# Optimization experiments

Hardware: AMD Instinct MI355X
Metric: run time of the kernel (lower is better)

Reference implementation:

```python
import jax, jax.numpy as jnp
import numpy as np

ALPHA = 1.0
BETA = 10.0
MARGIN = 0.5


def setup_inputs() -> dict:
    key = jax.random.key(0)
    k1, k2 = jax.random.split(key)
    emb = jax.random.normal(k1, (4096, 512), dtype=jnp.float32)
    # module docstring: embeddings are L2-normalized
    emb = emb / jnp.linalg.norm(emb, axis=1, keepdims=True)
    labels = jax.random.randint(k2, (4096,), 0, 64, dtype=jnp.int64)
    return {"embeddings": emb, "labels": labels}


def reference(embeddings, labels):
    n = embeddings.shape[0]
    sim = embeddings @ embeddings.T  # [n, n]
    labels_eq = labels[None, :] == labels[:, None]
    eye = jnp.eye(n, dtype=bool)
    pos_mask = labels_eq & ~eye
    neg_mask = ~labels_eq & ~eye

    # masked exp-sums (masked entries contribute 0, matching torch's
    # clone/NEG_INF/zero-out dance without materializing extra copies)
    pos_exp = jnp.where(pos_mask, jnp.exp(-ALPHA * (sim - MARGIN)), 0.0)
    neg_exp = jnp.where(neg_mask, jnp.exp(BETA * (sim - MARGIN)), 0.0)
    pos_term = (1.0 / ALPHA) * jnp.log1p(pos_exp.sum(axis=1))
    neg_term = (1.0 / BETA) * jnp.log1p(neg_exp.sum(axis=1))

    valid = pos_mask.any(axis=1) & neg_mask.any(axis=1)
    n_valid = valid.sum()
    total = jnp.where(valid, pos_term + neg_term, 0.0).sum()
    return jnp.where(n_valid > 0, total / jnp.maximum(n_valid, 1).astype(sim.dtype), 0.0)
```

## Files before the change

kernel.cpp:

```cpp
#include <hip/hip_runtime.h>
#include <hip/hip_bf16.h>

#define N 4096
#define D 512
#define MARGIN 0.5f
#define BETA 10.0f

typedef __attribute__((ext_vector_type(8))) short short8;
typedef __attribute__((ext_vector_type(4))) float floatx4;

__device__ inline unsigned short f2bf(float f) {
    unsigned u = __float_as_uint(f);
    u += 0x7fffu + ((u >> 16) & 1u);
    return (unsigned short)(u >> 16);
}

__global__ void convert_bf16_kernel(const float4* __restrict__ in,
                                    ushort4* __restrict__ out) {
    int idx = blockIdx.x * 256 + threadIdx.x;
    float4 v = in[idx];
    ushort4 o;
    o.x = f2bf(v.x); o.y = f2bf(v.y); o.z = f2bf(v.z); o.w = f2bf(v.w);
    out[idx] = o;
}

__global__ void ms_loss_gemm(const unsigned short* __restrict__ Ebf,
                             const int* __restrict__ labels,
                             float* __restrict__ pos_sum,
                             float* __restrict__ neg_sum) {
    __shared__ unsigned short Atile[128 * 32];
    __shared__ unsigned short Btile[128 * 32];
    __shared__ int rlab[128];
    __shared__ int clab[128];

    const int tid  = threadIdx.x;
    const int wave = tid >> 6;
    const int lane = tid & 63;
    const int quad = lane >> 4;
    const int lcol = lane & 15;
    const int wrow = wave >> 1;
    const int wcol = wave & 1;
    const int ibase = blockIdx.y * 128;
    const int jbase = blockIdx.x * 128;

    if (tid < 128)       rlab[tid]       = labels[ibase + tid];
    else                 clab[tid - 128] = labels[jbase + tid - 128];

    floatx4 acc[4][4];
#pragma unroll
    for (int mt = 0; mt < 4; ++mt)
#pragma unroll
        for (int nt = 0; nt < 4; ++nt)
            acc[mt][nt] = (floatx4){0.f, 0.f, 0.f, 0.f};

    const char* Eb = (const char*)Ebf;
    char* Ab = (char*)Atile;
    char* Bb = (char*)Btile;
    const int srow = lane >> 2;
    const int skb  = (lane & 3) * 16;

    for (int kt = 0; kt < D / 32; ++kt) {
        __syncthreads();
        const int kb = kt * 64;
#pragma unroll
        for (int it = 0; it < 2; ++it) {
            int r    = wave * 16 + it * 64 + srow;
            int ldso = wave * 1024 + it * 4096 + lane * 16;
            const char* ga = Eb + (size_t)(ibase + r) * (D * 2) + kb + skb;
            const char* gb = Eb + (size_t)(jbase + r) * (D * 2) + kb + skb;
            __builtin_amdgcn_global_load_lds(
                (const __attribute__((address_space(1))) void*)ga,
                (__attribute__((address_space(3))) void*)(Ab + ldso), 16, 0, 0);
            __builtin_amdgcn_global_load_lds(
                (const __attribute__((address_space(1))) void*)gb,
                (__attribute__((address_space(3))) void*)(Bb + ldso), 16, 0, 0);
        }
        __syncthreads();

        short8 a[4], b[4];
#pragma unroll
        for (int mt = 0; mt < 4; ++mt) {
            int r = wrow * 64 + mt * 16 + lcol;
            a[mt] = *(const short8*)(Ab + r * 64 + quad * 16);
        }
#pragma unroll
        for (int nt = 0; nt < 4; ++nt) {
            int c = wcol * 64 + nt * 16 + lcol;
            b[nt] = *(const short8*)(Bb + c * 64 + quad * 16);
        }
#pragma unroll
        for (int mt = 0; mt < 4; ++mt)
#pragma unroll
            for (int nt = 0; nt < 4; ++nt)
                acc[mt][nt] = __builtin_amdgcn_mfma_f32_16x16x32_bf16(
                    a[mt], b[nt], acc[mt][nt], 0, 0, 0);
    }

    float pacc[16], nacc[16];
#pragma unroll
    for (int t = 0; t < 16; ++t) { pacc[t] = 0.f; nacc[t] = 0.f; }

#pragma unroll
    for (int mt = 0; mt < 4; ++mt) {
#pragma unroll
        for (int nt = 0; nt < 4; ++nt) {
            int cl = wcol * 64 + nt * 16 + lcol;
            int gj = jbase + cl;
            int lj = clab[cl];
#pragma unroll
            for (int reg = 0; reg < 4; ++reg) {
                int rl = wrow * 64 + mt * 16 + quad * 4 + reg;
                int gi = ibase + rl;
                float s = acc[mt][nt][reg];
                if (gi != gj) {
                    if (rlab[rl] == lj)
                        pacc[mt * 4 + reg] += __expf(MARGIN - s);
                    else
                        nacc[mt * 4 + reg] += __expf(BETA * (s - MARGIN));
                }
            }
        }
    }

#pragma unroll
    for (int t = 0; t < 16; ++t) {
        float p = pacc[t], ng = nacc[t];
        p += __shfl_xor(p, 1);  ng += __shfl_xor(ng, 1);
        p += __shfl_xor(p, 2);  ng += __shfl_xor(ng, 2);
        p += __shfl_xor(p, 4);  ng += __shfl_xor(ng, 4);
        p += __shfl_xor(p, 8);  ng += __shfl_xor(ng, 8);
        if (lcol == 0) {
            int mt = t >> 2, reg = t & 3;
            int gi = ibase + wrow * 64 + mt * 16 + quad * 4 + reg;
            atomicAdd(&pos_sum[gi], p);
            atomicAdd(&neg_sum[gi], ng);
        }
    }
}

__global__ void finalize_kernel(const float* __restrict__ pos_sum,
                                const float* __restrict__ neg_sum,
                                float* __restrict__ out) {
    __shared__ float sb[256];
    __shared__ int   sc[256];
    const int tid = threadIdx.x;
    float tot = 0.f;
    int cnt = 0;
    for (int i = tid; i < N; i += 256) {
        float p = pos_sum[i], ng = neg_sum[i];
        if (p > 0.f && ng > 0.f) {
            tot += log1pf(p) + (1.0f / BETA) * log1pf(ng);
            cnt += 1;
        }
    }
    sb[tid] = tot; sc[tid] = cnt;
    __syncthreads();
    for (int s = 128; s > 0; s >>= 1) {
        if (tid < s) { sb[tid] += sb[tid + s]; sc[tid] += sc[tid + s]; }
        __syncthreads();
    }
    if (tid == 0) out[0] = (sc[0] > 0) ? sb[0] / (float)sc[0] : 0.f;
}

extern "C" void kernel_launch(void* const* d_in, const int* in_sizes, int n_in,
                              void* d_out, int out_size, void* d_ws, size_t ws_size,
                              hipStream_t stream) {
    const float* emb   = (const float*)d_in[0];
    const int* labels  = (const int*)d_in[1];
    float* out         = (float*)d_out;

    char* ws = (char*)d_ws;
    unsigned short* Ebf = (unsigned short*)ws;
    float* pos_sum = (float*)(ws + (size_t)N * D * 2);
    float* neg_sum = pos_sum + N;

    hipMemsetAsync(pos_sum, 0, 2 * N * sizeof(float), stream);

    convert_bf16_kernel<<<(N * D / 4) / 256, 256, 0, stream>>>(
        (const float4*)emb, (ushort4*)Ebf);

    dim3 grid(N / 128, N / 128);
    ms_loss_gemm<<<grid, 256, 0, stream>>>(Ebf, labels, pos_sum, neg_sum);

    finalize_kernel<<<1, 256, 0, stream>>>(pos_sum, neg_sum, out);
}
```

Measured before the change: 104.5 us.

## Swizzle LDS tiles, fuse zeroing into convert, restructure epilogue and finalize

XOR-swizzles the 16-byte k-chunks on both the global-to-LDS staging and the MFMA fragment reads, to reduce LDS bank conflicts. Drops the separate memset by zeroing the sum buffers inside the bf16 conversion kernel. Reorders the epilogue so each row's partial sums are reduced and committed right away instead of held in 32 accumulators, which lowers register pressure. Also adds launch bounds and vectorizes the finalize loads with float4.

```diff
diff --git a/kernel.cpp b/kernel.cpp
--- a/kernel.cpp
+++ b/kernel.cpp
@@ -15,19 +15,22 @@
     return (unsigned short)(u >> 16);
 }
 
-__global__ void convert_bf16_kernel(const float4* __restrict__ in,
-                                    ushort4* __restrict__ out) {
+__global__ __launch_bounds__(256) void convert_bf16_kernel(
+        const float4* __restrict__ in, ushort4* __restrict__ out,
+        float* __restrict__ sums ) {
     int idx = blockIdx.x * 256 + threadIdx.x;
+    if (idx < 2 * N) sums[idx] = 0.f;
     float4 v = in[idx];
     ushort4 o;
     o.x = f2bf(v.x); o.y = f2bf(v.y); o.z = f2bf(v.z); o.w = f2bf(v.w);
     out[idx] = o;
 }
 
-__global__ void ms_loss_gemm(const unsigned short* __restrict__ Ebf,
-                             const int* __restrict__ labels,
-                             float* __restrict__ pos_sum,
-                             float* __restrict__ neg_sum) {
+__global__ __launch_bounds__(256, 4) void ms_loss_gemm(
+        const unsigned short* __restrict__ Ebf,
+        const int* __restrict__ labels,
+        float* __restrict__ pos_sum,
+        float* __restrict__ neg_sum) {
     __shared__ unsigned short Atile[128 * 32];
     __shared__ unsigned short Btile[128 * 32];
     __shared__ int rlab[128];
@@ -57,7 +60,8 @@
     char* Ab = (char*)Atile;
     char* Bb = (char*)Btile;
     const int srow = lane >> 2;
-    const int skb  = (lane & 3) * 16;
+    const int sckb = ((lane & 3) ^ ((lane >> 3) & 3)) * 16;
+    const int rdsw = ((lcol >> 1) & 3);
 
     for (int kt = 0; kt < D / 32; ++kt) {
         __syncthreads();
@@ -66,8 +70,8 @@
         for (int it = 0; it < 2; ++it) {
             int r    = wave * 16 + it * 64 + srow;
             int ldso = wave * 1024 + it * 4096 + lane * 16;
-            const char* ga = Eb + (size_t)(ibase + r) * (D * 2) + kb + skb;
-            const char* gb = Eb + (size_t)(jbase + r) * (D * 2) + kb + skb;
+            const char* ga = Eb + (size_t)(ibase + r) * (D * 2) + kb + sckb;
+            const char* gb = Eb + (size_t)(jbase + r) * (D * 2) + kb + sckb;
             __builtin_amdgcn_global_load_lds(
                 (const __attribute__((address_space(1))) void*)ga,
                 (__attribute__((address_space(3))) void*)(Ab + ldso), 16, 0, 0);
@@ -78,15 +82,16 @@
         __syncthreads();
 
         short8 a[4], b[4];
+        const int rchunk = (quad ^ rdsw) * 16;
 #pragma unroll
         for (int mt = 0; mt < 4; ++mt) {
             int r = wrow * 64 + mt * 16 + lcol;
-            a[mt] = *(const short8*)(Ab + r * 64 + quad * 16);
+            a[mt] = *(const short8*)(Ab + r * 64 + rchunk);
         }
 #pragma unroll
         for (int nt = 0; nt < 4; ++nt) {
             int c = wcol * 64 + nt * 16 + lcol;
-            b[nt] = *(const short8*)(Bb + c * 64 + quad * 16);
+            b[nt] = *(const short8*)(Bb + c * 64 + rchunk);
         }
 #pragma unroll
         for (int mt = 0; mt < 4; ++mt)
@@ -96,61 +101,65 @@
                     a[mt], b[nt], acc[mt][nt], 0, 0, 0);
     }
 
-    float pacc[16], nacc[16];
+    int ljv[4], gjv[4];
 #pragma unroll
-    for (int t = 0; t < 16; ++t) { pacc[t] = 0.f; nacc[t] = 0.f; }
+    for (int nt = 0; nt < 4; ++nt) {
+        int cl = wcol * 64 + nt * 16 + lcol;
+        ljv[nt] = clab[cl];
+        gjv[nt] = jbase + cl;
+    }
 
 #pragma unroll
     for (int mt = 0; mt < 4; ++mt) {
 #pragma unroll
-        for (int nt = 0; nt < 4; ++nt) {
-            int cl = wcol * 64 + nt * 16 + lcol;
-            int gj = jbase + cl;
-            int lj = clab[cl];
+        for (int reg = 0; reg < 4; ++reg) {
+            int rl = wrow * 64 + mt * 16 + quad * 4 + reg;
+            int gi = ibase + rl;
+            int li = rlab[rl];
+            float p = 0.f, ng = 0.f;
 #pragma unroll
-            for (int reg = 0; reg < 4; ++reg) {
-                int rl = wrow * 64 + mt * 16 + quad * 4 + reg;
-                int gi = ibase + rl;
+            for (int nt = 0; nt < 4; ++nt) {
                 float s = acc[mt][nt][reg];
-                if (gi != gj) {
-                    if (rlab[rl] == lj)
-                        pacc[mt * 4 + reg] += __expf(MARGIN - s);
+                if (gi != gjv[nt]) {
+                    if (li == ljv[nt])
+                        p  += __expf(MARGIN - s);
                     else
-                        nacc[mt * 4 + reg] += __expf(BETA * (s - MARGIN));
+                        ng += __expf(BETA * (s - MARGIN));
                 }
             }
-        }
-    }
-
-#pragma unroll
-    for (int t = 0; t < 16; ++t) {
-        float p = pacc[t], ng = nacc[t];
-        p += __shfl_xor(p, 1);  ng += __shfl_xor(ng, 1);
-        p += __shfl_xor(p, 2);  ng += __shfl_xor(ng, 2);
-        p += __shfl_xor(p, 4);  ng += __shfl_xor(ng, 4);
-        p += __shfl_xor(p, 8);  ng += __shfl_xor(ng, 8);
-        if (lcol == 0) {
-            int mt = t >> 2, reg = t & 3;
-            int gi = ibase + wrow * 64 + mt * 16 + quad * 4 + reg;
-            atomicAdd(&pos_sum[gi], p);
-            atomicAdd(&neg_sum[gi], ng);
+            p  += __shfl_xor(p, 1);   ng += __shfl_xor(ng, 1);
+            p  += __shfl_xor(p, 2);   ng += __shfl_xor(ng, 2);
+            p  += __shfl_xor(p, 4);   ng += __shfl_xor(ng, 4);
+            p  += __shfl_xor(p, 8);   ng += __shfl_xor(ng, 8);
+            if (lcol == 0) {
+                atomicAdd(&pos_sum[gi], p);
+                atomicAdd(&neg_sum[gi], ng);
+            }
         }
     }
 }
 
-__global__ void finalize_kernel(const float* __restrict__ pos_sum,
-                                const float* __restrict__ neg_sum,
-                                float* __restrict__ out) {
+__global__ __launch_bounds__(256) void finalize_kernel(
+        const float4* __restrict__ pos4, const float4* __restrict__ neg4,
+        float* __restrict__ out) {
     __shared__ float sb[256];
     __shared__ int   sc[256];
     const int tid = threadIdx.x;
     float tot = 0.f;
     int cnt = 0;
-    for (int i = tid; i < N; i += 256) {
-        float p = pos_sum[i], ng = neg_sum[i];
-        if (p > 0.f && ng > 0.f) {
-            tot += log1pf(p) + (1.0f / BETA) * log1pf(ng);
-            cnt += 1;
+#pragma unroll
+    for (int it = 0; it < N / 4 / 256; ++it) {
+        int i = it * 256 + tid;
+        float4 p = pos4[i];
+        float4 ng = neg4[i];
+        const float* pp = (const float*)&p;
+        const float* nn = (const float*)&ng;
+#pragma unroll
+        for (int j = 0; j < 4; ++j) {
+            if (pp[j] > 0.f && nn[j] > 0.f) {
+                tot += log1pf(pp[j]) + (1.0f / BETA) * log1pf(nn[j]);
+                cnt += 1;
+            }
         }
     }
     sb[tid] = tot; sc[tid] = cnt;
@@ -174,13 +183,12 @@
     float* pos_sum = (float*)(ws + (size_t)N * D * 2);
     float* neg_sum = pos_sum + N;
 
-    hipMemsetAsync(pos_sum, 0, 2 * N * sizeof(float), stream);
-
     convert_bf16_kernel<<<(N * D / 4) / 256, 256, 0, stream>>>(
-        (const float4*)emb, (ushort4*)Ebf);
+        (const float4*)emb, (ushort4*)Ebf, pos_sum);
 
     dim3 grid(N / 128, N / 128);
     ms_loss_gemm<<<grid, 256, 0, stream>>>(Ebf, labels, pos_sum, neg_sum);
 
-    finalize_kernel<<<1, 256, 0, stream>>>(pos_sum, neg_sum, out);
+    finalize_kernel<<<1, 256, 0, stream>>>(
+        (const float4*)pos_sum, (const float4*)neg_sum, out);
 }
```

New measurement: 99.85 us. 1.05x faster.
